# Kernel optimization log

Measured on AMD Instinct MI355X. Metric: run time of the kernel, lower is better.

Reference implementation:

```python
import jax, jax.numpy as jnp
import numpy as np

U = 100000  # num_users
I = 100000  # num_items
D = 64      # dims
L = 50      # seq_L


def setup_inputs() -> dict:
    key = jax.random.key(0)
    ks = jax.random.split(key, 12)
    B, T = 4096, 100
    inp = {
        "user_ids": jax.random.randint(ks[0], (B,), 0, U),
        "item_seq_ids": jax.random.randint(ks[1], (B, L), 0, I),
        "target_item_ids": jax.random.randint(ks[2], (B, T), 0, I),
        # embedding tables (normal init)
        "user_table": jax.random.normal(ks[3], (U, D), jnp.float32) * 0.01,
        "item_table": jax.random.normal(ks[4], (I, D), jnp.float32) * 0.01,
        "W2_table": jax.random.normal(ks[5], (I, D), jnp.float32) * 0.01,
        "b2_table": jnp.zeros((I, 1), jnp.float32),
        # feature gates: Linear(dims, dims), he_uniform weight, zero bias
        "fg_item_W": jax.random.uniform(ks[6], (D, D), jnp.float32, -1.0, 1.0) * np.sqrt(6.0 / D),
        "fg_item_b": jnp.zeros((D,), jnp.float32),
        "fg_user_W": jax.random.uniform(ks[7], (D, D), jnp.float32, -1.0, 1.0) * np.sqrt(6.0 / D),
        "fg_user_b": jnp.zeros((D,), jnp.float32),
        # instance gates: xavier_uniform
        "inst_gate_item": jax.random.uniform(ks[8], (D, 1), jnp.float32, -1.0, 1.0) * np.sqrt(6.0 / (D + 1)),
        "inst_gate_user": jax.random.uniform(ks[9], (D, L), jnp.float32, -1.0, 1.0) * np.sqrt(6.0 / (D + L)),
    }
    return inp


def _forward_user(user_emb, item_embs, fg_item_W, fg_item_b, fg_user_W, fg_user_b,
                  inst_gate_item, inst_gate_user):
    # user_emb: [B,D], item_embs: [B,L,D]
    gate = jax.nn.sigmoid(
        item_embs @ fg_item_W.T + fg_item_b
        + (user_emb @ fg_user_W.T + fg_user_b)[:, None, :]
    )  # [B,L,D]
    gated = item_embs * gate  # [B,L,D]
    term1 = jnp.einsum("bld,d->bl", gated, inst_gate_item[:, 0])
    term2 = user_emb @ inst_gate_user  # [B,L]
    inst = jax.nn.sigmoid(term1 + term2)  # [B,L]
    union = jnp.sum(gated * inst[:, :, None], axis=1)  # [B,D]
    union = union / jnp.sum(inst, axis=1, keepdims=True)
    return union


def reference(user_ids, item_seq_ids, target_item_ids, user_table, item_table,
              W2_table, b2_table, fg_item_W, fg_item_b, fg_user_W, fg_user_b,
              inst_gate_item, inst_gate_user):
    item_embs = item_table[item_seq_ids]      # [B,L,D]
    user_emb = user_table[user_ids]           # [B,D]
    union = _forward_user(user_emb, item_embs, fg_item_W, fg_item_b,
                          fg_user_W, fg_user_b, inst_gate_item, inst_gate_user)
    w2 = W2_table[target_item_ids]            # [B,T,D]
    b2 = b2_table[target_item_ids][..., 0]    # [B,T]
    res = b2 + jnp.einsum("btd,bd->bt", w2, user_emb)
    res = res + jnp.einsum("bd,btd->bt", union, w2)
    # rel_score: bmm(item_embs, w2^T) summed over L == contract item_embs summed over L with w2
    res = res + jnp.einsum("bd,btd->bt", jnp.sum(item_embs, axis=1), w2)
    return res
```

## Files before the change

### kernel.cpp

```cpp
#include <hip/hip_runtime.h>

#define DD 64
#define LL 50
#define NB 4096
#define NT 100

typedef __attribute__((ext_vector_type(8))) __bf16 bf16x8;
typedef __attribute__((ext_vector_type(4))) float f32x4;

__device__ __forceinline__ float sigmoidf_(float x) {
    return __builtin_amdgcn_rcpf(1.0f + __expf(-x));
}
__device__ __forceinline__ unsigned pack_bf16(float hi, float lo) {
    union { float f; unsigned u; } a, b;
    a.f = hi; b.f = lo;
    return ((a.u + 0x8000u) & 0xffff0000u) | ((b.u + 0x8000u) >> 16);
}
__device__ __forceinline__ uint4 cvt8u(const float* f) {
    uint4 r;
    r.x = pack_bf16(f[1], f[0]);
    r.y = pack_bf16(f[3], f[2]);
    r.z = pack_bf16(f[5], f[4]);
    r.w = pack_bf16(f[7], f[6]);
    return r;
}
__device__ __forceinline__ bf16x8 cvt8(const float* f) {
    return __builtin_bit_cast(bf16x8, cvt8u(f));
}
__device__ __forceinline__ unsigned cvtpk(float lo, float hi) {
    unsigned r;
    asm("v_cvt_pk_bf16_f32 %0, %1, %2" : "=v"(r) : "v"(lo), "v"(hi));
    return r;
}
__device__ __forceinline__ bf16x8 cvt8f(const float* f) {
    uint4 r;
    r.x = cvtpk(f[0], f[1]);
    r.y = cvtpk(f[2], f[3]);
    r.z = cvtpk(f[4], f[5]);
    r.w = cvtpk(f[6], f[7]);
    return __builtin_bit_cast(bf16x8, r);
}
__device__ __forceinline__ void glds16(const float* g, float* l) {
    __builtin_amdgcn_global_load_lds(
        (const __attribute__((address_space(1))) void*)g,
        (__attribute__((address_space(3))) void*)l, 16, 0, 0);
}
__device__ __forceinline__ void glds4(const float* g, float* l) {
    __builtin_amdgcn_global_load_lds(
        (const __attribute__((address_space(1))) void*)g,
        (__attribute__((address_space(3))) void*)l, 4, 0, 0);
}

__global__ __launch_bounds__(128) void k0_user(
    const int* __restrict__ uid_g, const float* __restrict__ user_table,
    const float* __restrict__ Wu, const float* __restrict__ bu,
    const float* __restrict__ bi, const float* __restrict__ igu,
    const float* __restrict__ Wi,
    float* __restrict__ ufg_ws, float* __restrict__ t2_ws,
    unsigned short* __restrict__ wiB_ws)
{
    if (blockIdx.x == 256) {
        if (threadIdx.x >= 64) return;
        const int n = threadIdx.x;
        float tmp[64];
#pragma unroll
        for (int c4 = 0; c4 < 16; c4++)
            *(float4*)&tmp[c4 * 4] = *(const float4*)(Wi + n * DD + c4 * 4);
#pragma unroll
        for (int ch = 0; ch < 8; ch++)
            *(uint4*)(wiB_ws + n * DD + ch * 8) = cvt8u(tmp + ch * 8);
        return;
    }

    const int lane = threadIdx.x & 63;
    const int wv = threadIdx.x >> 6;
    const int c = lane & 15, q = lane >> 4;
    const int uid = uid_g[blockIdx.x * 16 + c];
    const float* urow = user_table + (size_t)uid * DD;

    bf16x8 af[2];
#pragma unroll
    for (int kf = 0; kf < 2; kf++) {
        float tmp[8];
        *(float4*)&tmp[0] = *(const float4*)(urow + kf * 32 + q * 8);
        *(float4*)&tmp[4] = *(const float4*)(urow + kf * 32 + q * 8 + 4);
        af[kf] = cvt8(tmp);
    }

#pragma unroll
    for (int ni0 = 0; ni0 < 4; ni0++) {
        const int ni = wv * 4 + ni0;
        f32x4 a = {0.f, 0.f, 0.f, 0.f};
#pragma unroll
        for (int kf = 0; kf < 2; kf++) {
            const int k0 = kf * 32 + q * 8;
            float tmp[8];
            if (ni < 4) {
                const float* src = Wu + (ni * 16 + c) * DD + k0;
                *(float4*)&tmp[0] = *(const float4*)src;
                *(float4*)&tmp[4] = *(const float4*)(src + 4);
            } else {
                const int l = ni * 16 + c - 64;
#pragma unroll
                for (int j = 0; j < 8; j++)
                    tmp[j] = (l < LL) ? igu[(k0 + j) * LL + l] : 0.f;
            }
            a = __builtin_amdgcn_mfma_f32_16x16x32_bf16(af[kf], cvt8(tmp), a, 0, 0, 0);
        }
        const int n = ni * 16 + c;
#pragma unroll
        for (int reg = 0; reg < 4; reg++) {
            const int bo = blockIdx.x * 16 + q * 4 + reg;
            if (n < DD)           ufg_ws[bo * DD + n] = a[reg] + bu[n] + bi[n];
            else if (n < DD + LL) t2_ws[bo * DD + (n - DD)] = a[reg];
        }
    }
}

__global__ __launch_bounds__(256, 4) void k1_fused(
    const int* __restrict__ uid_g, const int* __restrict__ iid_g,
    const int* __restrict__ tgt_g,
    const float* __restrict__ user_table, const float* __restrict__ item_table,
    const float* __restrict__ W2, const float* __restrict__ b2,
    const unsigned short* __restrict__ wiB, const float* __restrict__ igi,
    const float* __restrict__ ufg_ws, const float* __restrict__ t2_ws,
    float* __restrict__ out)
{
    const int tid = threadIdx.x;
    const int lane = tid & 63;
    const int w = tid >> 6;
    const int c = lane & 15, q = lane >> 4;
    const int j = tid & 15, gg = tid >> 4;
    const int b = blockIdx.x;

    __shared__ __align__(16) float sE[52 * DD];
    __shared__ __align__(16) float sT[DD];
    __shared__ __align__(16) float sB[128];
    __shared__ __align__(16) float sU[4 * DD];
    __shared__ __align__(16) float sS[4 * DD];
    __shared__ __align__(16) float sUu[DD];
    __shared__ float sI[4];
    __shared__ float sOut[112];

    const int* iidp = iid_g + b * LL;
    const int* tgtp = tgt_g + b * NT;

    int iid3[3];
#pragma unroll
    for (int k = 0; k < 3; k++) {
        const int s = w + 4 * k;
        const int r = 4 * s + (lane >> 4);
        iid3[k] = iidp[r < LL ? r : LL - 1];
    }
    int iid12 = 0;
    if (w == 0) {
        const int r = 48 + (lane >> 4);
        iid12 = iidp[r < LL ? r : LL - 1];
    }
#pragma unroll
    for (int k = 0; k < 3; k++) {
        const int s = w + 4 * k;
        const int r = 4 * s + (lane >> 4);
        const int j2 = (lane & 15) ^ (r & 7);
        glds16(item_table + (size_t)iid3[k] * DD + j2 * 4, sE + s * 256);
    }
    if (w == 0) {
        const int r = 48 + (lane >> 4);
        const int j2 = (lane & 15) ^ (r & 7);
        glds16(item_table + (size_t)iid12 * DD + j2 * 4, sE + 12 * 256);
    }

    if (w == 1)
        glds4(t2_ws + b * DD + (lane < LL ? lane : LL - 1), sT);
    if (w == 2) {
        const int tb = lane < NT ? lane : NT - 1;
        glds4(b2 + tgtp[tb], sB);
        const int uid = uid_g[b];
        glds4(user_table + (size_t)uid * DD + lane, sUu);
    }
    if (w == 3) {
        const int sl = 64 + lane;
        const int tb = sl < NT ? sl : NT - 1;
        glds4(b2 + tgtp[tb], sB + 64);
    }

    int tt[7];
#pragma unroll
    for (int i = 0; i < 7; i++) {
        const int ts = i * 16 + gg;
        tt[i] = tgtp[ts < NT ? ts : NT - 1];
    }
    float4 wv[7];
#pragma unroll
    for (int i = 0; i < 7; i++)
        wv[i] = *(const float4*)(W2 + (size_t)tt[i] * DD + j * 4);

    float ufg4[4], igi4[4];
#pragma unroll
    for (int ni = 0; ni < 4; ni++) {
        ufg4[ni] = ufg_ws[b * DD + ni * 16 + c];
        igi4[ni] = igi[ni * 16 + c];
    }

    __syncthreads();

    bf16x8 wb[4][2];
#pragma unroll
    for (int ni = 0; ni < 4; ni++)
#pragma unroll
        for (int kf = 0; kf < 2; kf++)
            wb[ni][kf] = __builtin_bit_cast(bf16x8,
                *(const uint4*)(wiB + (ni * 16 + c) * DD + kf * 32 + q * 8));

    bf16x8 ea[2];
    {
        const int row = w * 16 + c;
        const int rr = (row < LL) ? row : 0;
        const float* rowp = sE + rr * DD;
        const int s7 = rr & 7;
#pragma unroll
        for (int kf = 0; kf < 2; kf++) {
            float tmp[8];
            const int ch0 = (kf * 8 + 2 * q) ^ s7;
            const int ch1 = (kf * 8 + 2 * q + 1) ^ s7;
            *(float4*)&tmp[0] = *(const float4*)(rowp + ch0 * 4);
            *(float4*)&tmp[4] = *(const float4*)(rowp + ch1 * 4);
            if (row >= LL) {
#pragma unroll
                for (int i = 0; i < 8; i++) tmp[i] = 0.f;
            }
            ea[kf] = cvt8f(tmp);
        }
    }

    float unum[4] = {0.f, 0.f, 0.f, 0.f};
    float sip[4]  = {0.f, 0.f, 0.f, 0.f};
    float isum = 0.f;
    {
        f32x4 acc[4];
#pragma unroll
        for (int ni = 0; ni < 4; ni++) {
            f32x4 a = {0.f, 0.f, 0.f, 0.f};
            a = __builtin_amdgcn_mfma_f32_16x16x32_bf16(ea[0], wb[ni][0], a, 0, 0, 0);
            a = __builtin_amdgcn_mfma_f32_16x16x32_bf16(ea[1], wb[ni][1], a, 0, 0, 0);
            acc[ni] = a;
        }
#pragma unroll
        for (int reg = 0; reg < 4; reg++) {
            const int l = w * 16 + q * 4 + reg;
            const int valid = (l < LL);
            const int lr = valid ? l : 0;
            const int s7 = lr & 7;
            float gd[4];
            float t1 = 0.f;
#pragma unroll
            for (int ni = 0; ni < 4; ni++) {
                const int phys = (4 * ni + (c >> 2)) ^ s7;
                const float ev = sE[lr * DD + phys * 4 + (c & 3)];
                const float e = valid ? ev : 0.f;
                const float g = sigmoidf_(acc[ni][reg] + ufg4[ni]);
                gd[ni] = e * g;
                t1 += gd[ni] * igi4[ni];
                sip[ni] += e;
            }
            t1 += __shfl_xor(t1, 1); t1 += __shfl_xor(t1, 2);
            t1 += __shfl_xor(t1, 4); t1 += __shfl_xor(t1, 8);
            const float inst = valid ? sigmoidf_(t1 + sT[lr]) : 0.f;
            isum += inst;
#pragma unroll
            for (int ni = 0; ni < 4; ni++)
                unum[ni] += gd[ni] * inst;
        }
    }

#pragma unroll
    for (int ni = 0; ni < 4; ni++) {
        unum[ni] += __shfl_xor(unum[ni], 16); unum[ni] += __shfl_xor(unum[ni], 32);
        sip[ni]  += __shfl_xor(sip[ni], 16);  sip[ni]  += __shfl_xor(sip[ni], 32);
    }
    isum += __shfl_xor(isum, 16); isum += __shfl_xor(isum, 32);

    const float un = (q == 0) ? unum[0] : (q == 1) ? unum[1] : (q == 2) ? unum[2] : unum[3];
    const float si = (q == 0) ? sip[0]  : (q == 1) ? sip[1]  : (q == 2) ? sip[2]  : sip[3];
    sU[w * DD + lane] = un;
    sS[w * DD + lane] = si;
    if (lane == 0) sI[w] = isum;
    __syncthreads();

    float4 vr;
    {
        const float4 u0 = *(const float4*)&sU[0 * DD + j * 4];
        const float4 u1 = *(const float4*)&sU[1 * DD + j * 4];
        const float4 u2 = *(const float4*)&sU[2 * DD + j * 4];
        const float4 u3 = *(const float4*)&sU[3 * DD + j * 4];
        const float4 s0 = *(const float4*)&sS[0 * DD + j * 4];
        const float4 s1 = *(const float4*)&sS[1 * DD + j * 4];
        const float4 s2 = *(const float4*)&sS[2 * DD + j * 4];
        const float4 s3 = *(const float4*)&sS[3 * DD + j * 4];
        const float4 uu = *(const float4*)&sUu[j * 4];
        const float rist = __builtin_amdgcn_rcpf(sI[0] + sI[1] + sI[2] + sI[3]);
        vr.x = uu.x + (u0.x + u1.x + u2.x + u3.x) * rist + (s0.x + s1.x + s2.x + s3.x);
        vr.y = uu.y + (u0.y + u1.y + u2.y + u3.y) * rist + (s0.y + s1.y + s2.y + s3.y);
        vr.z = uu.z + (u0.z + u1.z + u2.z + u3.z) * rist + (s0.z + s1.z + s2.z + s3.z);
        vr.w = uu.w + (u0.w + u1.w + u2.w + u3.w) * rist + (s0.w + s1.w + s2.w + s3.w);
    }

#pragma unroll
    for (int i = 0; i < 7; i++) {
        const int ts = i * 16 + gg;
        float s = wv[i].x * vr.x + wv[i].y * vr.y + wv[i].z * vr.z + wv[i].w * vr.w;
        s += __shfl_xor(s, 1); s += __shfl_xor(s, 2);
        s += __shfl_xor(s, 4); s += __shfl_xor(s, 8);
        if (j == 0 && ts < NT) sOut[ts] = s + sB[ts];
    }
    __syncthreads();
    if (tid < NT) out[b * NT + tid] = sOut[tid];
}

extern "C" void kernel_launch(void* const* d_in, const int* in_sizes, int n_in,
                              void* d_out, int out_size, void* d_ws, size_t ws_size,
                              hipStream_t stream)
{
    const int* user_ids        = (const int*)d_in[0];
    const int* item_seq_ids    = (const int*)d_in[1];
    const int* target_item_ids = (const int*)d_in[2];
    const float* user_tab      = (const float*)d_in[3];
    const float* item_tab      = (const float*)d_in[4];
    const float* W2_tab        = (const float*)d_in[5];
    const float* b2_tab        = (const float*)d_in[6];
    const float* fg_item_W     = (const float*)d_in[7];
    const float* fg_item_b     = (const float*)d_in[8];
    const float* fg_user_W     = (const float*)d_in[9];
    const float* fg_user_b     = (const float*)d_in[10];
    const float* igi           = (const float*)d_in[11];
    const float* igu           = (const float*)d_in[12];
    float* out = (float*)d_out;

    float* ufg_ws = (float*)d_ws;
    float* t2_ws  = ufg_ws + NB * DD;
    unsigned short* wiB_ws = (unsigned short*)(t2_ws + NB * DD);

    k0_user<<<257, 128, 0, stream>>>(user_ids, user_tab, fg_user_W, fg_user_b,
                                     fg_item_b, igu, fg_item_W,
                                     ufg_ws, t2_ws, wiB_ws);
    k1_fused<<<NB, 256, 0, stream>>>(user_ids, item_seq_ids, target_item_ids,
                                     user_tab, item_tab, W2_tab, b2_tab,
                                     wiB_ws, igi, ufg_ws, t2_ws, out);
}
```

Measured before the change: 154.6 us.

## Give each wave private item-row LDS slice and drop the block barrier

```diff
diff --git a/kernel.cpp b/kernel.cpp
--- a/kernel.cpp
+++ b/kernel.cpp
@@ -133,50 +133,50 @@
     const int j = tid & 15, gg = tid >> 4;
     const int b = blockIdx.x;
 
-    __shared__ __align__(16) float sE[52 * DD];
-    __shared__ __align__(16) float sT[DD];
+    __shared__ __align__(16) float sE[4][16 * DD];
     __shared__ __align__(16) float sB[128];
+    __shared__ __align__(16) float sUu[DD];
     __shared__ __align__(16) float sU[4 * DD];
     __shared__ __align__(16) float sS[4 * DD];
-    __shared__ __align__(16) float sUu[DD];
     __shared__ float sI[4];
     __shared__ float sOut[112];
 
     const int* iidp = iid_g + b * LL;
     const int* tgtp = tgt_g + b * NT;
-
-    int iid3[3];
-#pragma unroll
-    for (int k = 0; k < 3; k++) {
-        const int s = w + 4 * k;
-        const int r = 4 * s + (lane >> 4);
-        iid3[k] = iidp[r < LL ? r : LL - 1];
-    }
-    int iid12 = 0;
-    if (w == 0) {
-        const int r = 48 + (lane >> 4);
-        iid12 = iidp[r < LL ? r : LL - 1];
-    }
-#pragma unroll
-    for (int k = 0; k < 3; k++) {
-        const int s = w + 4 * k;
-        const int r = 4 * s + (lane >> 4);
-        const int j2 = (lane & 15) ^ (r & 7);
-        glds16(item_table + (size_t)iid3[k] * DD + j2 * 4, sE + s * 256);
-    }
-    if (w == 0) {
-        const int r = 48 + (lane >> 4);
-        const int j2 = (lane & 15) ^ (r & 7);
-        glds16(item_table + (size_t)iid12 * DD + j2 * 4, sE + 12 * 256);
-    }
-
-    if (w == 1)
-        glds4(t2_ws + b * DD + (lane < LL ? lane : LL - 1), sT);
+    float* sEw = sE[w];
+
+    int iid4[4];
+#pragma unroll
+    for (int s = 0; s < 4; s++) {
+        const int r = w * 16 + 4 * s + (lane >> 4);
+        iid4[s] = iidp[r < LL ? r : LL - 1];
+    }
+    int tt[7];
+#pragma unroll
+    for (int i = 0; i < 7; i++) {
+        const int ts = i * 16 + gg;
+        tt[i] = tgtp[ts < NT ? ts : NT - 1];
+    }
+
+#pragma unroll
+    for (int s = 0; s < 4; s++) {
+        const int rl = 4 * s + (lane >> 4);
+        const int j2 = (lane & 15) ^ (rl & 7);
+        glds16(item_table + (size_t)iid4[s] * DD + j2 * 4, sEw + s * 256);
+    }
+
+    float4 wv[7];
+#pragma unroll
+    for (int i = 0; i < 7; i++)
+        wv[i] = *(const float4*)(W2 + (size_t)tt[i] * DD + j * 4);
+
+    if (w == 1) {
+        const int uid = uid_g[b];
+        glds4(user_table + (size_t)uid * DD + lane, sUu);
+    }
     if (w == 2) {
         const int tb = lane < NT ? lane : NT - 1;
         glds4(b2 + tgtp[tb], sB);
-        const int uid = uid_g[b];
-        glds4(user_table + (size_t)uid * DD + lane, sUu);
     }
     if (w == 3) {
         const int sl = 64 + lane;
@@ -184,25 +184,14 @@
         glds4(b2 + tgtp[tb], sB + 64);
     }
 
-    int tt[7];
-#pragma unroll
-    for (int i = 0; i < 7; i++) {
-        const int ts = i * 16 + gg;
-        tt[i] = tgtp[ts < NT ? ts : NT - 1];
-    }
-    float4 wv[7];
-#pragma unroll
-    for (int i = 0; i < 7; i++)
-        wv[i] = *(const float4*)(W2 + (size_t)tt[i] * DD + j * 4);
-
     float ufg4[4], igi4[4];
 #pragma unroll
     for (int ni = 0; ni < 4; ni++) {
         ufg4[ni] = ufg_ws[b * DD + ni * 16 + c];
         igi4[ni] = igi[ni * 16 + c];
     }
-
-    __syncthreads();
+    const float4 t2v = *(const float4*)(t2_ws + b * DD + w * 16 + q * 4);
+    float t2a[4] = {t2v.x, t2v.y, t2v.z, t2v.w};
 
     bf16x8 wb[4][2];
 #pragma unroll
@@ -212,12 +201,14 @@
             wb[ni][kf] = __builtin_bit_cast(bf16x8,
                 *(const uint4*)(wiB + (ni * 16 + c) * DD + kf * 32 + q * 8));
 
+    asm volatile("s_waitcnt vmcnt(0)" ::: "memory");
+    __builtin_amdgcn_sched_barrier(0);
+
     bf16x8 ea[2];
     {
-        const int row = w * 16 + c;
-        const int rr = (row < LL) ? row : 0;
-        const float* rowp = sE + rr * DD;
-        const int s7 = rr & 7;
+        const int grow = w * 16 + c;
+        const float* rowp = sEw + c * DD;
+        const int s7 = c & 7;
 #pragma unroll
         for (int kf = 0; kf < 2; kf++) {
             float tmp[8];
@@ -225,7 +216,7 @@
             const int ch1 = (kf * 8 + 2 * q + 1) ^ s7;
             *(float4*)&tmp[0] = *(const float4*)(rowp + ch0 * 4);
             *(float4*)&tmp[4] = *(const float4*)(rowp + ch1 * 4);
-            if (row >= LL) {
+            if (grow >= LL) {
 #pragma unroll
                 for (int i = 0; i < 8; i++) tmp[i] = 0.f;
             }
@@ -247,16 +238,15 @@
         }
 #pragma unroll
         for (int reg = 0; reg < 4; reg++) {
-            const int l = w * 16 + q * 4 + reg;
-            const int valid = (l < LL);
-            const int lr = valid ? l : 0;
-            const int s7 = lr & 7;
+            const int lrl = q * 4 + reg;
+            const int valid = (w * 16 + lrl < LL);
+            const int s7 = lrl & 7;
             float gd[4];
             float t1 = 0.f;
 #pragma unroll
             for (int ni = 0; ni < 4; ni++) {
                 const int phys = (4 * ni + (c >> 2)) ^ s7;
-                const float ev = sE[lr * DD + phys * 4 + (c & 3)];
+                const float ev = sEw[lrl * DD + phys * 4 + (c & 3)];
                 const float e = valid ? ev : 0.f;
                 const float g = sigmoidf_(acc[ni][reg] + ufg4[ni]);
                 gd[ni] = e * g;
@@ -265,7 +255,7 @@
             }
             t1 += __shfl_xor(t1, 1); t1 += __shfl_xor(t1, 2);
             t1 += __shfl_xor(t1, 4); t1 += __shfl_xor(t1, 8);
-            const float inst = valid ? sigmoidf_(t1 + sT[lr]) : 0.f;
+            const float inst = valid ? sigmoidf_(t1 + t2a[reg]) : 0.f;
             isum += inst;
 #pragma unroll
             for (int ni = 0; ni < 4; ni++)
```

Measured after the change: 153.6 us. Within noise of the previous version (-0.6%).
